# Performance work log

Hardware: AMD Instinct MI355X
Metric: run time of the kernel (lower is better)

## Reference

```python
import jax, jax.numpy as jnp
import numpy as np

NUM_CLASSES = 100000
EMBED = 512
BATCH = 4096
LAMBDA = 0.01
ALPHA = 0.1


def setup_inputs() -> dict:
    key = jax.random.key(0)
    k1, k2, k3 = jax.random.split(key, 3)
    y = jax.random.randint(k1, (BATCH,), 0, NUM_CLASSES, dtype=jnp.int64 if jax.config.jax_enable_x64 else jnp.int32)
    batch = jax.random.normal(k2, (BATCH, EMBED), dtype=jnp.float32)
    centers = jax.random.normal(k3, (NUM_CLASSES, EMBED), dtype=jnp.float32)
    return {"y": y, "batch": batch, "centers": centers}


def reference(y, batch, centers):
    # gather per-sample class centers: [B, E]
    centers_pred = centers[y]
    delta = batch - centers_pred  # gradient does NOT flow through centers_pred in torch (Variable(..., requires_grad=False))
    # training-mode sparse scatter-add update; duplicate indices accumulate (torch sparse add semantics)
    new_centers = centers.at[y].add(ALPHA * jax.lax.stop_gradient(delta))
    b = jnp.asarray(BATCH, dtype=delta.dtype)
    loss = LAMBDA * jnp.sum(jnp.sum(delta * delta, axis=1) / b)
    return loss, new_centers
```

## Files before the change

### kernel.cpp

```cpp
#include <hip/hip_runtime.h>


constexpr int   NUM_CLASSES = 100000;
constexpr int   EMBED       = 512;
constexpr int   BATCH       = 4096;
constexpr float LAMBDA      = 0.01f;
constexpr float ALPHA       = 0.1f;

constexpr long  NFLOAT = (long)NUM_CLASSES * EMBED;
constexpr long  NGRP   = (NFLOAT - 3) / 4;
constexpr long  NSRC4  = NFLOAT / 4;
constexpr int   NWAVES_UPD = 4096;

typedef float f4 __attribute__((ext_vector_type(4)));

__global__ void init_head_kernel(int* __restrict__ head) {
    int c = blockIdx.x * blockDim.x + threadIdx.x;
    if (c < NUM_CLASSES) head[c] = -1;
}

__global__ void link_kernel(const int* __restrict__ y, int* __restrict__ head,
                            int* __restrict__ nxt) {
    int s = blockIdx.x * blockDim.x + threadIdx.x;
    if (s < BATCH) nxt[s] = atomicExch(&head[y[s]], s);
}

__global__ void __launch_bounds__(256) copy_shift_kernel(
        const f4* __restrict__ src4, f4* __restrict__ dst4,
        const float* __restrict__ src, float* __restrict__ dst) {
    const int  lane = threadIdx.x & 63;
    const long gw   = (long)((blockIdx.x * blockDim.x + threadIdx.x) >> 6);
    const long nw   = (long)((gridDim.x * blockDim.x) >> 6);

    for (long base = gw * 64; base < NGRP; base += nw * 64) {
        const long g  = base + lane;
        f4 v = (g < NSRC4) ? src4[g] : (f4){0.f, 0.f, 0.f, 0.f};

        f4 vn;
        vn.x = __shfl_down(v.x, 1, 64);
        vn.y = __shfl_down(v.y, 1, 64);
        vn.z = __shfl_down(v.z, 1, 64);
        vn.w = __shfl_down(v.w, 1, 64);
        if (lane == 63 && g + 1 < NSRC4) vn = src4[g + 1];

        if (g < NGRP) {
            f4 o = {v.w, vn.x, vn.y, vn.z};
            __builtin_nontemporal_store(o, &dst4[1 + g]);
        }
    }

    if (blockIdx.x == 0 && threadIdx.x == 0) {
        dst[1] = src[0];
        dst[2] = src[1];
        dst[3] = src[2];
        dst[NFLOAT] = src[NFLOAT - 1];
    }
}

__global__ void __launch_bounds__(256) update_rows_kernel(
        const float* __restrict__ batch,
        const float* __restrict__ centers,
        const int* __restrict__ head,
        const int* __restrict__ nxt,
        float* __restrict__ out,
        float* __restrict__ loss_part) {
    const int lane = threadIdx.x & 63;
    const int wid  = threadIdx.x >> 6;
    const int gw   = blockIdx.x * 4 + wid;
    const int nw   = gridDim.x * 4;

    float lacc = 0.f;
    for (int r = gw; r < NUM_CLASSES; r += nw) {
        int s = head[r];
        if (s < 0) continue;

        const float* crow = centers + (size_t)r * EMBED;
        float c[8], a[8];
        #pragma unroll
        for (int k = 0; k < 8; ++k) { c[k] = crow[lane + 64 * k]; a[k] = 0.f; }

        while (s >= 0) {
            const float* brow = batch + (size_t)s * EMBED;
            #pragma unroll
            for (int k = 0; k < 8; ++k) {
                float d = brow[lane + 64 * k] - c[k];
                a[k] += d;
                lacc += d * d;
            }
            s = nxt[s];
        }

        float* orow = out + 1 + (size_t)r * EMBED;
        #pragma unroll
        for (int k = 0; k < 8; ++k) orow[lane + 64 * k] = c[k] + ALPHA * a[k];
    }

    #pragma unroll
    for (int off = 32; off > 0; off >>= 1) lacc += __shfl_xor(lacc, off, 64);
    if (lane == 0) loss_part[gw] = lacc;
}

__global__ void __launch_bounds__(1024) reduce_loss_kernel(
        const float* __restrict__ loss_part, float* __restrict__ out) {
    const int t = threadIdx.x;
    float v = loss_part[t] + loss_part[t + 1024] +
              loss_part[t + 2048] + loss_part[t + 3072];
    #pragma unroll
    for (int off = 32; off > 0; off >>= 1) v += __shfl_xor(v, off, 64);

    __shared__ float wsum[16];
    const int lane = t & 63, wid = t >> 6;
    if (lane == 0) wsum[wid] = v;
    __syncthreads();
    if (t == 0) {
        float s = 0.f;
        #pragma unroll
        for (int i = 0; i < 16; ++i) s += wsum[i];
        out[0] = s * (LAMBDA / (float)BATCH);
    }
}

__global__ void center_update_fallback(const int* __restrict__ y,
                                       const float4* __restrict__ batch,
                                       const float4* __restrict__ centers,
                                       float* __restrict__ out) {
    const int b = blockIdx.x, t = threadIdx.x;
    const int cls = y[b];
    const float4 xb = batch[(size_t)b * (EMBED / 4) + t];
    const float4 c  = centers[(size_t)cls * (EMBED / 4) + t];
    const float dx = xb.x - c.x, dy = xb.y - c.y, dz = xb.z - c.z, dw = xb.w - c.w;
    float* orow = out + 1 + (size_t)cls * EMBED + (size_t)t * 4;
    atomicAdd(orow + 0, ALPHA * dx);
    atomicAdd(orow + 1, ALPHA * dy);
    atomicAdd(orow + 2, ALPHA * dz);
    atomicAdd(orow + 3, ALPHA * dw);
    float s = dx * dx + dy * dy + dz * dz + dw * dw;
    #pragma unroll
    for (int off = 32; off > 0; off >>= 1) s += __shfl_down(s, off, 64);
    __shared__ float wsum[2];
    const int lane = t & 63, wid = t >> 6;
    if (lane == 0) wsum[wid] = s;
    __syncthreads();
    if (t == 0) atomicAdd(out, (wsum[0] + wsum[1]) * (LAMBDA / (float)BATCH));
}

extern "C" void kernel_launch(void* const* d_in, const int* in_sizes, int n_in,
                              void* d_out, int out_size, void* d_ws, size_t ws_size,
                              hipStream_t stream) {
    const int*   y       = (const int*)d_in[0];
    const float* batch   = (const float*)d_in[1];
    const float* centers = (const float*)d_in[2];
    float*       out     = (float*)d_out;

    const size_t head_bytes = (size_t)NUM_CLASSES * sizeof(int);
    const size_t next_bytes = (size_t)BATCH * sizeof(int);
    const size_t loss_bytes = (size_t)NWAVES_UPD * sizeof(float);

    if (ws_size >= head_bytes + next_bytes + loss_bytes) {
        int*   head      = (int*)d_ws;
        int*   nxt       = (int*)((char*)d_ws + head_bytes);
        float* loss_part = (float*)((char*)d_ws + head_bytes + next_bytes);

        init_head_kernel<<<(NUM_CLASSES + 1023) / 1024, 1024, 0, stream>>>(head);
        link_kernel<<<(BATCH + 255) / 256, 256, 0, stream>>>(y, head, nxt);
        copy_shift_kernel<<<2048, 256, 0, stream>>>(
            (const f4*)centers, (f4*)out, centers, out);
        update_rows_kernel<<<1024, 256, 0, stream>>>(batch, centers, head, nxt,
                                                     out, loss_part);
        reduce_loss_kernel<<<1, 1024, 0, stream>>>(loss_part, out);
    } else {
        (void)hipMemsetAsync(out, 0, sizeof(float), stream);
        (void)hipMemcpyAsync(out + 1, centers, NFLOAT * sizeof(float),
                             hipMemcpyDeviceToDevice, stream);
        center_update_fallback<<<BATCH, EMBED / 4, 0, stream>>>(
            y, (const float4*)batch, (const float4*)centers, out);
    }
}
```

Baseline: 87.13 us.

## Fuse center copy-shift and row update into one per-row kernel

Replaces the separate full-table shifted copy kernel and the sparse row-update kernel with a single kernel where each wave loads its whole center row once as float4, applies any linked batch updates, and writes the row shifted by one float using wave shuffles and nontemporal stores. This removes the second pass over updated rows and the write-after-write ordering between the two kernels. It also removes one kernel launch. The grid grows to 2048 blocks and the loss partial buffer to 8192 entries. Edge floats are handled with per-lane scalar stores, which adds some divergent writes.

```diff
diff --git a/kernel.cpp b/kernel.cpp
--- a/kernel.cpp
+++ b/kernel.cpp
@@ -8,9 +8,7 @@
 constexpr float ALPHA       = 0.1f;
 
 constexpr long  NFLOAT = (long)NUM_CLASSES * EMBED;
-constexpr long  NGRP   = (NFLOAT - 3) / 4;
-constexpr long  NSRC4  = NFLOAT / 4;
-constexpr int   NWAVES_UPD = 4096;
+constexpr int   NWAVES = 8192;
 
 typedef float f4 __attribute__((ext_vector_type(4)));
 
@@ -25,44 +23,14 @@
     if (s < BATCH) nxt[s] = atomicExch(&head[y[s]], s);
 }
 
-__global__ void __launch_bounds__(256) copy_shift_kernel(
-        const f4* __restrict__ src4, f4* __restrict__ dst4,
-        const float* __restrict__ src, float* __restrict__ dst) {
-    const int  lane = threadIdx.x & 63;
-    const long gw   = (long)((blockIdx.x * blockDim.x + threadIdx.x) >> 6);
-    const long nw   = (long)((gridDim.x * blockDim.x) >> 6);
-
-    for (long base = gw * 64; base < NGRP; base += nw * 64) {
-        const long g  = base + lane;
-        f4 v = (g < NSRC4) ? src4[g] : (f4){0.f, 0.f, 0.f, 0.f};
-
-        f4 vn;
-        vn.x = __shfl_down(v.x, 1, 64);
-        vn.y = __shfl_down(v.y, 1, 64);
-        vn.z = __shfl_down(v.z, 1, 64);
-        vn.w = __shfl_down(v.w, 1, 64);
-        if (lane == 63 && g + 1 < NSRC4) vn = src4[g + 1];
-
-        if (g < NGRP) {
-            f4 o = {v.w, vn.x, vn.y, vn.z};
-            __builtin_nontemporal_store(o, &dst4[1 + g]);
-        }
-    }
-
-    if (blockIdx.x == 0 && threadIdx.x == 0) {
-        dst[1] = src[0];
-        dst[2] = src[1];
-        dst[3] = src[2];
-        dst[NFLOAT] = src[NFLOAT - 1];
-    }
-}
-
-__global__ void __launch_bounds__(256) update_rows_kernel(
-        const float* __restrict__ batch,
-        const float* __restrict__ centers,
+__global__ void __launch_bounds__(256) fused_rows_kernel(
+        const f4* __restrict__ src4,
+        const f4* __restrict__ batch4,
+        f4* __restrict__ dst4,
+        const float* __restrict__ src,
+        float* __restrict__ dst,
         const int* __restrict__ head,
         const int* __restrict__ nxt,
-        float* __restrict__ out,
         float* __restrict__ loss_part) {
     const int lane = threadIdx.x & 63;
     const int wid  = threadIdx.x >> 6;
@@ -71,28 +39,54 @@
 
     float lacc = 0.f;
     for (int r = gw; r < NUM_CLASSES; r += nw) {
+        const long base = 128L * r;
+        f4 c0 = src4[base + lane];
+        f4 c1 = src4[base + 64 + lane];
+
         int s = head[r];
-        if (s < 0) continue;
-
-        const float* crow = centers + (size_t)r * EMBED;
-        float c[8], a[8];
-        #pragma unroll
-        for (int k = 0; k < 8; ++k) { c[k] = crow[lane + 64 * k]; a[k] = 0.f; }
-
-        while (s >= 0) {
-            const float* brow = batch + (size_t)s * EMBED;
-            #pragma unroll
-            for (int k = 0; k < 8; ++k) {
-                float d = brow[lane + 64 * k] - c[k];
-                a[k] += d;
-                lacc += d * d;
-            }
-            s = nxt[s];
+        if (s >= 0) {
+            f4 a0 = {0.f, 0.f, 0.f, 0.f}, a1 = a0;
+            do {
+                const long bb = 128L * s;
+                f4 b0 = batch4[bb + lane];
+                f4 b1 = batch4[bb + 64 + lane];
+                f4 d0 = b0 - c0;
+                f4 d1 = b1 - c1;
+                a0 += d0;
+                a1 += d1;
+                lacc += d0.x * d0.x + d0.y * d0.y + d0.z * d0.z + d0.w * d0.w
+                      + d1.x * d1.x + d1.y * d1.y + d1.z * d1.z + d1.w * d1.w;
+                s = nxt[s];
+            } while (s >= 0);
+            c0 += ALPHA * a0;
+            c1 += ALPHA * a1;
         }
 
-        float* orow = out + 1 + (size_t)r * EMBED;
-        #pragma unroll
-        for (int k = 0; k < 8; ++k) orow[lane + 64 * k] = c[k] + ALPHA * a[k];
+        float c1x0 = __shfl(c1.x, 0, 64);
+        float c1y0 = __shfl(c1.y, 0, 64);
+        float c1z0 = __shfl(c1.z, 0, 64);
+        float n0x = __shfl_down(c0.x, 1, 64);
+        float n0y = __shfl_down(c0.y, 1, 64);
+        float n0z = __shfl_down(c0.z, 1, 64);
+        float n1x = __shfl_down(c1.x, 1, 64);
+        float n1y = __shfl_down(c1.y, 1, 64);
+        float n1z = __shfl_down(c1.z, 1, 64);
+        if (lane == 63) { n0x = c1x0; n0y = c1y0; n0z = c1z0; }
+
+        f4 o0 = {c0.w, n0x, n0y, n0z};
+        __builtin_nontemporal_store(o0, &dst4[base + 1 + lane]);
+        if (lane < 63) {
+            f4 o1 = {c1.w, n1x, n1y, n1z};
+            __builtin_nontemporal_store(o1, &dst4[base + 65 + lane]);
+        }
+        if (lane == 0) {
+            dst[1 + 512L * r] = c0.x;
+            dst[2 + 512L * r] = c0.y;
+            dst[3 + 512L * r] = c0.z;
+        }
+        if (lane == 63) {
+            dst[512L * r + 512] = c1.w;
+        }
     }
 
     #pragma unroll
@@ -103,8 +97,9 @@
 __global__ void __launch_bounds__(1024) reduce_loss_kernel(
         const float* __restrict__ loss_part, float* __restrict__ out) {
     const int t = threadIdx.x;
-    float v = loss_part[t] + loss_part[t + 1024] +
-              loss_part[t + 2048] + loss_part[t + 3072];
+    float v = 0.f;
+    #pragma unroll
+    for (int k = 0; k < NWAVES / 1024; ++k) v += loss_part[t + k * 1024];
     #pragma unroll
     for (int off = 32; off > 0; off >>= 1) v += __shfl_xor(v, off, 64);
 
@@ -154,7 +149,7 @@
 
     const size_t head_bytes = (size_t)NUM_CLASSES * sizeof(int);
     const size_t next_bytes = (size_t)BATCH * sizeof(int);
-    const size_t loss_bytes = (size_t)NWAVES_UPD * sizeof(float);
+    const size_t loss_bytes = (size_t)NWAVES * sizeof(float);
 
     if (ws_size >= head_bytes + next_bytes + loss_bytes) {
         int*   head      = (int*)d_ws;
@@ -163,10 +158,9 @@
 
         init_head_kernel<<<(NUM_CLASSES + 1023) / 1024, 1024, 0, stream>>>(head);
         link_kernel<<<(BATCH + 255) / 256, 256, 0, stream>>>(y, head, nxt);
-        copy_shift_kernel<<<2048, 256, 0, stream>>>(
-            (const f4*)centers, (f4*)out, centers, out);
-        update_rows_kernel<<<1024, 256, 0, stream>>>(batch, centers, head, nxt,
-                                                     out, loss_part);
+        fused_rows_kernel<<<2048, 256, 0, stream>>>(
+            (const f4*)centers, (const f4*)batch, (f4*)out,
+            centers, out, head, nxt, loss_part);
         reduce_loss_kernel<<<1, 1024, 0, stream>>>(loss_part, out);
     } else {
         (void)hipMemsetAsync(out, 0, sizeof(float), stream);
```

Result: faster. 79.62 us (-8.6%).
